# Kernel optimization log

Hardware: AMD Instinct MI355X
Metric: run time of the kernel (lower is better)

Reference implementation:

```python
import jax, jax.numpy as jnp
import numpy as np

N_NODES = 100000
N_EDGES = 800000
F_IN = 58


def setup_inputs() -> dict:
    key = jax.random.key(0)
    ks = jax.random.split(key, 8)
    x = jax.random.normal(ks[0], (N_NODES, F_IN), dtype=jnp.float32)
    edge_index = jax.random.randint(ks[1], (2, N_EDGES), 0, N_NODES, dtype=jnp.int64)

    def glorot(k, shape):
        fan_in = shape[-2]
        return jax.random.normal(k, shape, dtype=jnp.float32) * (1.0 / np.sqrt(fan_in))

    W1 = glorot(ks[2], (2, 58, 300))
    b1 = jnp.zeros((300,), jnp.float32)
    W2 = glorot(ks[3], (2, 300, 100))
    b2 = jnp.zeros((100,), jnp.float32)
    W3 = glorot(ks[4], (2, 100, 1))
    b3 = jnp.zeros((1,), jnp.float32)
    return {"x": x, "edge_index": edge_index, "W1": W1, "b1": b1,
            "W2": W2, "b2": b2, "W3": W3, "b3": b3}


def cheb_conv_k2(x, edge_index, W, b):
    """PyG ChebConv, K=2, sym normalization, lambda_max=2:
    L_hat = -D^{-1/2} A D^{-1/2}; out = x @ W[0] + (L_hat x) @ W[1] + b."""
    src, dst = edge_index[0], edge_index[1]
    n = x.shape[0]
    ones = jnp.ones(src.shape, x.dtype)
    deg = jax.ops.segment_sum(ones, src, num_segments=n)  # degree from row index
    dinv = jnp.where(deg > 0, 1.0 / jnp.sqrt(jnp.where(deg > 0, deg, 1.0)), 0.0)
    w = -(dinv[src] * dinv[dst])                          # [E] edge weights of L_hat
    tx1 = jax.ops.segment_sum(w[:, None] * x[src], dst, num_segments=n)  # [N,F]
    return x @ W[0] + tx1 @ W[1] + b


def reference(x, edge_index, W1, b1, W2, b2, W3, b3):
    # eval mode: dropout layers are identity
    h = jax.nn.relu(cheb_conv_k2(x, edge_index, W1, b1))
    h = jax.nn.relu(cheb_conv_k2(h, edge_index, W2, b2))
    return cheb_conv_k2(h, edge_index, W3, b3)
```

## Files before the change

### kernel.cpp

```cpp
#include <hip/hip_runtime.h>


typedef short bf16x8 __attribute__((ext_vector_type(8)));
typedef float f32x4 __attribute__((ext_vector_type(4)));

__device__ __forceinline__ unsigned f2bf(float f) {
  unsigned u = __float_as_uint(f);
  u += 0x7fff + ((u >> 16) & 1);
  return u >> 16;
}
__device__ __forceinline__ float bf2f(unsigned s) {
  return __uint_as_float(s << 16);
}

__global__ void k_count(const int* __restrict__ src, const int* __restrict__ dst,
                        unsigned* __restrict__ deg, unsigned* __restrict__ cnt,
                        unsigned* __restrict__ rank, int E) {
  int i = blockIdx.x * blockDim.x + threadIdx.x;
  if (i < E) {
    atomicAdd(&deg[src[i]], 1u);
    rank[i] = atomicAdd(&cnt[dst[i]], 1u);
  }
}

__global__ void k_dinv(const unsigned* __restrict__ deg, float* __restrict__ dinv, int N) {
  int i = blockIdx.x * blockDim.x + threadIdx.x;
  if (i < N) {
    unsigned d = deg[i];
    dinv[i] = d ? rsqrtf((float)d) : 0.0f;
  }
}

__global__ __launch_bounds__(256) void k_scan1(const unsigned* __restrict__ cnt,
                                               unsigned* __restrict__ btot, int N) {
  __shared__ unsigned s[256];
  int b = blockIdx.x, t = threadIdx.x;
  int base = b * 1024;
  unsigned sum = 0;
  for (int i = t; i < 1024; i += 256) {
    int idx = base + i;
    sum += (idx < N) ? cnt[idx] : 0u;
  }
  s[t] = sum;
  __syncthreads();
  for (int off = 128; off > 0; off >>= 1) {
    if (t < off) s[t] += s[t + off];
    __syncthreads();
  }
  if (t == 0) btot[b] = s[0];
}

__global__ __launch_bounds__(256) void k_scan2(unsigned* __restrict__ btot,
                                               unsigned* __restrict__ rowstart,
                                               int NB, int N, int E) {
  __shared__ unsigned s[256];
  int t = threadIdx.x;
  s[t] = (t < NB) ? btot[t] : 0u;
  __syncthreads();
  if (t == 0) {
    unsigned acc = 0;
    for (int i = 0; i < NB; i++) { unsigned v = s[i]; s[i] = acc; acc += v; }
  }
  __syncthreads();
  if (t < NB) btot[t] = s[t];
  if (t == 0) rowstart[N] = (unsigned)E;
}

__global__ __launch_bounds__(256) void k_scan3(const unsigned* __restrict__ cnt,
                                               const unsigned* __restrict__ btot,
                                               unsigned* __restrict__ rowstart, int N) {
  __shared__ unsigned ssum[256];
  int b = blockIdx.x, t = threadIdx.x;
  int base = b * 1024 + t * 4;
  unsigned v0 = 0, v1 = 0, v2 = 0, v3 = 0;
  if (base + 0 < N) v0 = cnt[base + 0];
  if (base + 1 < N) v1 = cnt[base + 1];
  if (base + 2 < N) v2 = cnt[base + 2];
  if (base + 3 < N) v3 = cnt[base + 3];
  ssum[t] = v0 + v1 + v2 + v3;
  __syncthreads();
  for (int off = 1; off < 256; off <<= 1) {
    unsigned add = (t >= off) ? ssum[t - off] : 0u;
    __syncthreads();
    ssum[t] += add;
    __syncthreads();
  }
  unsigned texcl = ((t == 0) ? 0u : ssum[t - 1]) + btot[b];
  unsigned r0 = texcl, r1 = r0 + v0, r2 = r1 + v1, r3 = r2 + v2;
  if (base + 0 < N) rowstart[base + 0] = r0;
  if (base + 1 < N) rowstart[base + 1] = r1;
  if (base + 2 < N) rowstart[base + 2] = r2;
  if (base + 3 < N) rowstart[base + 3] = r3;
}

__global__ void k_fill(const int* __restrict__ src, const int* __restrict__ dst,
                       const float* __restrict__ dinv, const unsigned* __restrict__ rowstart,
                       const unsigned* __restrict__ rank, int2* __restrict__ er, int E) {
  int e = blockIdx.x * blockDim.x + threadIdx.x;
  if (e >= E) return;
  int s = src[e], d = dst[e];
  er[rowstart[d] + rank[e]] = make_int2(s, __float_as_int(dinv[s]));
}

__global__ void k_prep_xb(const float* __restrict__ x, unsigned short* __restrict__ xb, int N) {
  int idx = blockIdx.x * blockDim.x + threadIdx.x;
  int n = idx >> 6, p = idx & 63;
  if (n >= N) return;
  int c = p * 2;
  if (c < 58) {
    unsigned lo = f2bf(x[(size_t)n * 58 + c]);
    unsigned hi = f2bf(x[(size_t)n * 58 + c + 1]);
    *(unsigned*)(xb + (size_t)n * 128 + c) = lo | (hi << 16);
  } else if (c >= 116) {
    *(unsigned*)(xb + (size_t)n * 128 + c) = 0;
  }
}

__global__ void k_prep_w1f(const float* __restrict__ W1, uint4* __restrict__ W1f) {
  int idx = blockIdx.x * blockDim.x + threadIdx.x;
  if (idx >= 4 * 20 * 64) return;
  int lane = idx & 63, j = (idx >> 6) % 20, s = (idx >> 6) / 20;
  int lr = lane & 15, g = lane >> 4;
  int c = j * 16 + lr;
  unsigned short v[8];
#pragma unroll
  for (int i = 0; i < 8; i++) {
    int k = s * 32 + g * 8 + i;
    float f = 0.0f;
    if (c < 300 && k < 116)
      f = (k < 58) ? W1[k * 300 + c] : W1[17400 + (k - 58) * 300 + c];
    v[i] = (unsigned short)f2bf(f);
  }
  W1f[idx] = *(const uint4*)v;
}

__global__ void k_prep_w2f(const float* __restrict__ W2, uint4* __restrict__ W2f) {
  int idx = blockIdx.x * blockDim.x + threadIdx.x;
  if (idx >= 10 * 13 * 64) return;
  int lane = idx & 63, j = (idx >> 6) % 13, s = (idx >> 6) / 13;
  int lr = lane & 15, g = lane >> 4;
  int r = j * 16 + lr;
  unsigned short v[8];
#pragma unroll
  for (int i = 0; i < 8; i++) {
    int k = s * 32 + g * 8 + i;
    float f = 0.0f;
    if (k < 300) {
      if (r < 100) f = W2[30000 + k * 100 + r];
      else if (r >= 104 && r < 204) f = W2[k * 100 + (r - 104)];
    }
    v[i] = (unsigned short)f2bf(f);
  }
  W2f[idx] = *(const uint4*)v;
}

__global__ void k_prep_b1pad(const float* __restrict__ b1, float* __restrict__ b1pad) {
  int t = blockIdx.x * blockDim.x + threadIdx.x;
  if (t < 320) b1pad[t] = (t < 300) ? b1[t] : 0.0f;
}

__global__ __launch_bounds__(256) void k_gather58(
    const unsigned* __restrict__ rowstart, const int2* __restrict__ er,
    const float* __restrict__ dinv, unsigned short* __restrict__ xb, int N) {
  int wid = (blockIdx.x * blockDim.x + threadIdx.x) >> 6;
  if (wid >= N) return;
  int lane = threadIdx.x & 63;
  int c0 = lane * 2;
  if (c0 >= 58) return;
  unsigned s0 = rowstart[wid], s1 = rowstart[wid + 1];
  float a0 = 0.f, a1 = 0.f, b0 = 0.f, b1 = 0.f;
  float c0a = 0.f, c1a = 0.f, d0 = 0.f, d1 = 0.f;
  unsigned e = s0;
  for (; e + 4 <= s1; e += 4) {
    int2 r0 = er[e], r1 = er[e + 1], r2 = er[e + 2], r3 = er[e + 3];
    unsigned v0 = *(const unsigned*)(xb + (size_t)r0.x * 128 + c0);
    unsigned v1 = *(const unsigned*)(xb + (size_t)r1.x * 128 + c0);
    unsigned v2 = *(const unsigned*)(xb + (size_t)r2.x * 128 + c0);
    unsigned v3 = *(const unsigned*)(xb + (size_t)r3.x * 128 + c0);
    float w0 = __int_as_float(r0.y), w1 = __int_as_float(r1.y);
    float w2 = __int_as_float(r2.y), w3 = __int_as_float(r3.y);
    a0 += w0 * bf2f(v0 & 0xffffu); a1 += w0 * bf2f(v0 >> 16);
    b0 += w1 * bf2f(v1 & 0xffffu); b1 += w1 * bf2f(v1 >> 16);
    c0a += w2 * bf2f(v2 & 0xffffu); c1a += w2 * bf2f(v2 >> 16);
    d0 += w3 * bf2f(v3 & 0xffffu); d1 += w3 * bf2f(v3 >> 16);
  }
  for (; e < s1; ++e) {
    int2 r = er[e];
    float w = __int_as_float(r.y);
    unsigned v = *(const unsigned*)(xb + (size_t)r.x * 128 + c0);
    a0 += w * bf2f(v & 0xffffu); a1 += w * bf2f(v >> 16);
  }
  float dd = -dinv[wid];
  float p0 = dd * ((a0 + b0) + (c0a + d0));
  float p1 = dd * ((a1 + b1) + (c1a + d1));
  *(unsigned*)(xb + (size_t)wid * 128 + 58 + c0) = f2bf(p0) | (f2bf(p1) << 16);
}

__global__ __launch_bounds__(256) void k_gather_l2(
    const unsigned* __restrict__ rowstart, const int2* __restrict__ er,
    const float* __restrict__ dinv, const unsigned short* __restrict__ ga2b,
    const float* __restrict__ b2, const float* __restrict__ W30,
    const float* __restrict__ W31, const float* __restrict__ b3,
    float* __restrict__ a3, float* __restrict__ g3, int N) {
  int wid = (blockIdx.x * blockDim.x + threadIdx.x) >> 6;
  if (wid >= N) return;
  int lane = threadIdx.x & 63;
  int c0 = lane * 2;
  bool act = c0 < 100;
  unsigned s0 = rowstart[wid], s1 = rowstart[wid + 1];
  float aa = 0.f, gg = 0.f;
  if (act) {
    float a0 = 0.f, a1 = 0.f, b0 = 0.f, b1 = 0.f;
    float c0a = 0.f, c1a = 0.f, d0 = 0.f, d1 = 0.f;
    unsigned e = s0;
    for (; e + 4 <= s1; e += 4) {
      int2 r0 = er[e], r1 = er[e + 1], r2 = er[e + 2], r3 = er[e + 3];
      unsigned v0 = *(const unsigned*)(ga2b + (size_t)r0.x * 208 + c0);
      unsigned v1 = *(const unsigned*)(ga2b + (size_t)r1.x * 208 + c0);
      unsigned v2 = *(const unsigned*)(ga2b + (size_t)r2.x * 208 + c0);
      unsigned v3 = *(const unsigned*)(ga2b + (size_t)r3.x * 208 + c0);
      float w0 = __int_as_float(r0.y), w1 = __int_as_float(r1.y);
      float w2 = __int_as_float(r2.y), w3 = __int_as_float(r3.y);
      a0 += w0 * bf2f(v0 & 0xffffu); a1 += w0 * bf2f(v0 >> 16);
      b0 += w1 * bf2f(v1 & 0xffffu); b1 += w1 * bf2f(v1 >> 16);
      c0a += w2 * bf2f(v2 & 0xffffu); c1a += w2 * bf2f(v2 >> 16);
      d0 += w3 * bf2f(v3 & 0xffffu); d1 += w3 * bf2f(v3 >> 16);
    }
    for (; e < s1; ++e) {
      int2 r = er[e];
      float w = __int_as_float(r.y);
      unsigned v = *(const unsigned*)(ga2b + (size_t)r.x * 208 + c0);
      a0 += w * bf2f(v & 0xffffu); a1 += w * bf2f(v >> 16);
    }
    float dd = -dinv[wid];
    float p0 = dd * ((a0 + b0) + (c0a + d0));
    float p1 = dd * ((a1 + b1) + (c1a + d1));
    unsigned av = *(const unsigned*)(ga2b + (size_t)wid * 208 + 104 + c0);
    float h0 = fmaxf(bf2f(av & 0xffffu) + p0 + b2[c0], 0.f);
    float h1 = fmaxf(bf2f(av >> 16) + p1 + b2[c0 + 1], 0.f);
    aa = h0 * W30[c0] + h1 * W30[c0 + 1];
    gg = h0 * W31[c0] + h1 * W31[c0 + 1];
  }
#pragma unroll
  for (int off = 32; off > 0; off >>= 1) {
    aa += __shfl_xor(aa, off);
    gg += __shfl_xor(gg, off);
  }
  if (lane == 0) {
    a3[wid] = aa + b3[0];
    g3[wid] = gg;
  }
}

__global__ void k_gather1(const unsigned* __restrict__ rowstart, const int2* __restrict__ er,
                          const float* __restrict__ dinv, const float* __restrict__ g3,
                          const float* __restrict__ a3, float* __restrict__ out, int N) {
  int n = blockIdx.x * blockDim.x + threadIdx.x;
  if (n >= N) return;
  unsigned s0 = rowstart[n], s1 = rowstart[n + 1];
  float a = 0.f, b = 0.f, c = 0.f, d = 0.f;
  unsigned e = s0;
  for (; e + 4 <= s1; e += 4) {
    int2 r0 = er[e], r1 = er[e + 1], r2 = er[e + 2], r3 = er[e + 3];
    float g0 = g3[r0.x], g1 = g3[r1.x], g2v = g3[r2.x], g3v = g3[r3.x];
    a += __int_as_float(r0.y) * g0;
    b += __int_as_float(r1.y) * g1;
    c += __int_as_float(r2.y) * g2v;
    d += __int_as_float(r3.y) * g3v;
  }
  for (; e < s1; ++e) {
    int2 r = er[e];
    a += __int_as_float(r.y) * g3[r.x];
  }
  out[n] = a3[n] - dinv[n] * ((a + b) + (c + d));
}

#define STG 324
__global__ __launch_bounds__(256, 3) void k_mm12_mfma(
    const unsigned short* __restrict__ xb, const uint4* __restrict__ W1f,
    const uint4* __restrict__ W2f, const float* __restrict__ b1pad,
    unsigned short* __restrict__ ga2b) {
  __shared__ unsigned short stage[4 * 16 * STG];
  int tid = threadIdx.x;
  int lane = tid & 63, wv = tid >> 6, lr = lane & 15, g = lane >> 4;
  int n0 = blockIdx.x * 64 + wv * 16;
  unsigned short* ost = stage + wv * 16 * STG;

  bf16x8 a1[4];
#pragma unroll
  for (int s = 0; s < 4; s++)
    a1[s] = *(const bf16x8*)(xb + (size_t)(n0 + lr) * 128 + s * 32 + g * 8);
#pragma unroll
  for (int half = 0; half < 2; half++) {
    f32x4 acc[10];
#pragma unroll
    for (int j = 0; j < 10; j++) acc[j] = (f32x4){0.f, 0.f, 0.f, 0.f};
#pragma unroll
    for (int s = 0; s < 4; s++) {
      bf16x8 w[10];
#pragma unroll
      for (int j = 0; j < 10; j++)
        w[j] = *(const bf16x8*)&W1f[(s * 20 + half * 10 + j) * 64 + lane];
      __builtin_amdgcn_sched_barrier(0);
#pragma unroll
      for (int j = 0; j < 10; j++)
        acc[j] = __builtin_amdgcn_mfma_f32_16x16x32_bf16(w[j], a1[s], acc[j], 0, 0, 0);
    }
#pragma unroll
    for (int j = 0; j < 10; j++) {
      int c = half * 160 + j * 16 + g * 4;
      float4 bv = *(const float4*)(b1pad + c);
      unsigned lo = f2bf(fmaxf(acc[j][0] + bv.x, 0.f)) |
                    (f2bf(fmaxf(acc[j][1] + bv.y, 0.f)) << 16);
      unsigned hi = f2bf(fmaxf(acc[j][2] + bv.z, 0.f)) |
                    (f2bf(fmaxf(acc[j][3] + bv.w, 0.f)) << 16);
      uint2 pk; pk.x = lo; pk.y = hi;
      *(uint2*)(ost + lr * STG + c) = pk;
    }
  }

  uint2 pk0[7], pk1[6];
  {
    f32x4 acc[7];
#pragma unroll
    for (int j = 0; j < 7; j++) acc[j] = (f32x4){0.f, 0.f, 0.f, 0.f};
#pragma unroll
    for (int s = 0; s < 10; s++) {
      bf16x8 a = *(const bf16x8*)(ost + lr * STG + s * 32 + g * 8);
      bf16x8 w[7];
#pragma unroll
      for (int j = 0; j < 7; j++) w[j] = *(const bf16x8*)&W2f[(s * 13 + j) * 64 + lane];
      __builtin_amdgcn_sched_barrier(0);
#pragma unroll
      for (int j = 0; j < 7; j++)
        acc[j] = __builtin_amdgcn_mfma_f32_16x16x32_bf16(w[j], a, acc[j], 0, 0, 0);
    }
#pragma unroll
    for (int j = 0; j < 7; j++) {
      pk0[j].x = f2bf(acc[j][0]) | (f2bf(acc[j][1]) << 16);
      pk0[j].y = f2bf(acc[j][2]) | (f2bf(acc[j][3]) << 16);
    }
  }
  {
    f32x4 acc[6];
#pragma unroll
    for (int j = 0; j < 6; j++) acc[j] = (f32x4){0.f, 0.f, 0.f, 0.f};
#pragma unroll
    for (int s = 0; s < 10; s++) {
      bf16x8 a = *(const bf16x8*)(ost + lr * STG + s * 32 + g * 8);
      bf16x8 w[6];
#pragma unroll
      for (int j = 0; j < 6; j++) w[j] = *(const bf16x8*)&W2f[(s * 13 + 7 + j) * 64 + lane];
      __builtin_amdgcn_sched_barrier(0);
#pragma unroll
      for (int j = 0; j < 6; j++)
        acc[j] = __builtin_amdgcn_mfma_f32_16x16x32_bf16(w[j], a, acc[j], 0, 0, 0);
    }
#pragma unroll
    for (int j = 0; j < 6; j++) {
      pk1[j].x = f2bf(acc[j][0]) | (f2bf(acc[j][1]) << 16);
      pk1[j].y = f2bf(acc[j][2]) | (f2bf(acc[j][3]) << 16);
    }
  }
#pragma unroll
  for (int j = 0; j < 7; j++)
    *(uint2*)(ost + lr * 216 + j * 16 + g * 4) = pk0[j];
#pragma unroll
  for (int j = 0; j < 6; j++)
    *(uint2*)(ost + lr * 216 + (7 + j) * 16 + g * 4) = pk1[j];
  uint4* gdst = (uint4*)(ga2b + (size_t)n0 * 208);
  for (int idx = lane; idx < 416; idx += 64) {
    int row = idx / 26, q = idx - row * 26;
    gdst[idx] = *(const uint4*)(ost + row * 216 + q * 8);
  }
}

extern "C" void kernel_launch(void* const* d_in, const int* in_sizes, int n_in,
                              void* d_out, int out_size, void* d_ws, size_t ws_size,
                              hipStream_t stream) {
  const float* x  = (const float*)d_in[0];
  const int*   ei = (const int*)d_in[1];
  const float* W1 = (const float*)d_in[2];
  const float* b1 = (const float*)d_in[3];
  const float* W2 = (const float*)d_in[4];
  const float* b2 = (const float*)d_in[5];
  const float* W3 = (const float*)d_in[6];
  const float* b3 = (const float*)d_in[7];
  float* out = (float*)d_out;

  const int N = in_sizes[0] / 58;
  const int E = in_sizes[1] / 2;
  const int NR = (N + 127) & ~127;
  const int NB = (N + 1023) / 1024;
  const int* src = ei;
  const int* dst = ei + E;

  char* ws = (char*)d_ws;
  size_t off = 0;
  auto alloc = [&](size_t bytes) -> void* {
    void* p = ws + off;
    off += (bytes + 255) & ~(size_t)255;
    return p;
  };
  unsigned* deg      = (unsigned*)alloc((size_t)2 * N * 4);
  unsigned* cnt      = deg + N;
  float*    dinv     = (float*)alloc((size_t)N * 4);
  unsigned* rowstart = (unsigned*)alloc((size_t)(N + 1) * 4);
  unsigned* rank     = (unsigned*)alloc((size_t)E * 4);
  unsigned* btot     = (unsigned*)alloc((size_t)256 * 4);
  int2*     er       = (int2*)alloc((size_t)E * 8);
  unsigned short* xb   = (unsigned short*)alloc((size_t)NR * 128 * 2);
  uint4*    W1f      = (uint4*)alloc((size_t)4 * 20 * 64 * 16);
  uint4*    W2f      = (uint4*)alloc((size_t)10 * 13 * 64 * 16);
  float*    b1pad    = (float*)alloc((size_t)320 * 4);
  unsigned short* ga2b = (unsigned short*)alloc((size_t)NR * 208 * 2);
  float* a3 = (float*)alloc((size_t)N * 4);
  float* g3 = (float*)alloc((size_t)N * 4);

  hipMemsetAsync(deg, 0, (size_t)2 * N * 4, stream);
  k_count<<<(E + 255) / 256, 256, 0, stream>>>(src, dst, deg, cnt, rank, E);
  k_dinv<<<(N + 255) / 256, 256, 0, stream>>>(deg, dinv, N);
  k_scan1<<<NB, 256, 0, stream>>>(cnt, btot, N);
  k_scan2<<<1, 256, 0, stream>>>(btot, rowstart, NB, N, E);
  k_scan3<<<NB, 256, 0, stream>>>(cnt, btot, rowstart, N);
  k_fill<<<(E + 255) / 256, 256, 0, stream>>>(src, dst, dinv, rowstart, rank, er, E);

  k_prep_w1f<<<(4 * 20 * 64 + 255) / 256, 256, 0, stream>>>(W1, W1f);
  k_prep_w2f<<<(10 * 13 * 64 + 255) / 256, 256, 0, stream>>>(W2, W2f);
  k_prep_b1pad<<<2, 256, 0, stream>>>(b1, b1pad);
  k_prep_xb<<<((size_t)N * 64 + 255) / 256, 256, 0, stream>>>(x, xb, N);

  k_gather58<<<(N + 3) / 4, 256, 0, stream>>>(rowstart, er, dinv, xb, N);
  k_mm12_mfma<<<NR / 64, 256, 0, stream>>>(xb, W1f, W2f, b1pad, ga2b);
  k_gather_l2<<<(N + 3) / 4, 256, 0, stream>>>(rowstart, er, dinv, ga2b,
                                               b2, W3, W3 + 100, b3, a3, g3, N);

  k_gather1<<<(N + 255) / 256, 256, 0, stream>>>(rowstart, er, dinv, g3, a3, out, N);
}
```

Before: 304.9 us.

## Fuse prep kernels into count launch, pack two nodes per wave, deepen gather unroll

The edge counting, x bf16 conversion, weight repacking and bias padding kernels are merged into one launch that dispatches on block ranges, removing several launch gaps. The 58-column gather now handles two nodes per 64-lane wave using half-waves, so fewer lanes sit idle. All three gather kernels switch to an 8-way unrolled edge loop with clamped indices and zeroed weights on the tail, giving more loads in flight per lane. The trade-offs are wasted loads on the padded tail slots and higher register pressure.

```diff
diff --git a/kernel.cpp b/kernel.cpp
--- a/kernel.cpp
+++ b/kernel.cpp
@@ -13,13 +13,81 @@
   return __uint_as_float(s << 16);
 }
 
-__global__ void k_count(const int* __restrict__ src, const int* __restrict__ dst,
-                        unsigned* __restrict__ deg, unsigned* __restrict__ cnt,
-                        unsigned* __restrict__ rank, int E) {
-  int i = blockIdx.x * blockDim.x + threadIdx.x;
-  if (i < E) {
-    atomicAdd(&deg[src[i]], 1u);
-    rank[i] = atomicAdd(&cnt[dst[i]], 1u);
+__global__ void k_count_prep(
+    const int* __restrict__ src, const int* __restrict__ dst,
+    unsigned* __restrict__ deg, unsigned* __restrict__ cnt,
+    unsigned* __restrict__ rank, int E, int EB,
+    const float* __restrict__ x, unsigned short* __restrict__ xb, int N, int XB,
+    const float* __restrict__ W1, uint4* __restrict__ W1f,
+    const float* __restrict__ W2, uint4* __restrict__ W2f,
+    const float* __restrict__ b1, float* __restrict__ b1pad) {
+  int b = blockIdx.x, t = threadIdx.x;
+  if (b < EB) {
+    int i = b * 256 + t;
+    if (i < E) {
+      atomicAdd(&deg[src[i]], 1u);
+      rank[i] = atomicAdd(&cnt[dst[i]], 1u);
+    }
+    return;
+  }
+  b -= EB;
+  if (b < XB) {
+    int idx = b * 256 + t;
+    int n = idx >> 6, p = idx & 63;
+    if (n >= N) return;
+    int c = p * 2;
+    if (c < 58) {
+      unsigned lo = f2bf(x[(size_t)n * 58 + c]);
+      unsigned hi = f2bf(x[(size_t)n * 58 + c + 1]);
+      *(unsigned*)(xb + (size_t)n * 128 + c) = lo | (hi << 16);
+    } else if (c >= 116) {
+      *(unsigned*)(xb + (size_t)n * 128 + c) = 0;
+    }
+    return;
+  }
+  b -= XB;
+  if (b < 20) {
+    int idx = b * 256 + t;
+    int lane = idx & 63, j = (idx >> 6) % 20, s = (idx >> 6) / 20;
+    int lr = lane & 15, g = lane >> 4;
+    int c = j * 16 + lr;
+    unsigned short v[8];
+#pragma unroll
+    for (int i = 0; i < 8; i++) {
+      int k = s * 32 + g * 8 + i;
+      float f = 0.0f;
+      if (c < 300 && k < 116)
+        f = (k < 58) ? W1[k * 300 + c] : W1[17400 + (k - 58) * 300 + c];
+      v[i] = (unsigned short)f2bf(f);
+    }
+    W1f[idx] = *(const uint4*)v;
+    return;
+  }
+  b -= 20;
+  if (b < 33) {
+    int idx = b * 256 + t;
+    if (idx >= 10 * 13 * 64) return;
+    int lane = idx & 63, j = (idx >> 6) % 13, s = (idx >> 6) / 13;
+    int lr = lane & 15, g = lane >> 4;
+    int r = j * 16 + lr;
+    unsigned short v[8];
+#pragma unroll
+    for (int i = 0; i < 8; i++) {
+      int k = s * 32 + g * 8 + i;
+      float f = 0.0f;
+      if (k < 300) {
+        if (r < 100) f = W2[30000 + k * 100 + r];
+        else if (r >= 104 && r < 204) f = W2[k * 100 + (r - 104)];
+      }
+      v[i] = (unsigned short)f2bf(f);
+    }
+    W2f[idx] = *(const uint4*)v;
+    return;
+  }
+  b -= 33;
+  {
+    int idx = b * 256 + t;
+    if (idx < 320) b1pad[idx] = (idx < 300) ? b1[idx] : 0.0f;
   }
 }
 
@@ -102,97 +170,39 @@
   er[rowstart[d] + rank[e]] = make_int2(s, __float_as_int(dinv[s]));
 }
 
-__global__ void k_prep_xb(const float* __restrict__ x, unsigned short* __restrict__ xb, int N) {
-  int idx = blockIdx.x * blockDim.x + threadIdx.x;
-  int n = idx >> 6, p = idx & 63;
-  if (n >= N) return;
-  int c = p * 2;
-  if (c < 58) {
-    unsigned lo = f2bf(x[(size_t)n * 58 + c]);
-    unsigned hi = f2bf(x[(size_t)n * 58 + c + 1]);
-    *(unsigned*)(xb + (size_t)n * 128 + c) = lo | (hi << 16);
-  } else if (c >= 116) {
-    *(unsigned*)(xb + (size_t)n * 128 + c) = 0;
-  }
-}
-
-__global__ void k_prep_w1f(const float* __restrict__ W1, uint4* __restrict__ W1f) {
-  int idx = blockIdx.x * blockDim.x + threadIdx.x;
-  if (idx >= 4 * 20 * 64) return;
-  int lane = idx & 63, j = (idx >> 6) % 20, s = (idx >> 6) / 20;
-  int lr = lane & 15, g = lane >> 4;
-  int c = j * 16 + lr;
-  unsigned short v[8];
-#pragma unroll
-  for (int i = 0; i < 8; i++) {
-    int k = s * 32 + g * 8 + i;
-    float f = 0.0f;
-    if (c < 300 && k < 116)
-      f = (k < 58) ? W1[k * 300 + c] : W1[17400 + (k - 58) * 300 + c];
-    v[i] = (unsigned short)f2bf(f);
-  }
-  W1f[idx] = *(const uint4*)v;
-}
-
-__global__ void k_prep_w2f(const float* __restrict__ W2, uint4* __restrict__ W2f) {
-  int idx = blockIdx.x * blockDim.x + threadIdx.x;
-  if (idx >= 10 * 13 * 64) return;
-  int lane = idx & 63, j = (idx >> 6) % 13, s = (idx >> 6) / 13;
-  int lr = lane & 15, g = lane >> 4;
-  int r = j * 16 + lr;
-  unsigned short v[8];
-#pragma unroll
-  for (int i = 0; i < 8; i++) {
-    int k = s * 32 + g * 8 + i;
-    float f = 0.0f;
-    if (k < 300) {
-      if (r < 100) f = W2[30000 + k * 100 + r];
-      else if (r >= 104 && r < 204) f = W2[k * 100 + (r - 104)];
-    }
-    v[i] = (unsigned short)f2bf(f);
-  }
-  W2f[idx] = *(const uint4*)v;
-}
-
-__global__ void k_prep_b1pad(const float* __restrict__ b1, float* __restrict__ b1pad) {
-  int t = blockIdx.x * blockDim.x + threadIdx.x;
-  if (t < 320) b1pad[t] = (t < 300) ? b1[t] : 0.0f;
-}
-
 __global__ __launch_bounds__(256) void k_gather58(
     const unsigned* __restrict__ rowstart, const int2* __restrict__ er,
     const float* __restrict__ dinv, unsigned short* __restrict__ xb, int N) {
-  int wid = (blockIdx.x * blockDim.x + threadIdx.x) >> 6;
-  if (wid >= N) return;
+  int pair = (blockIdx.x * blockDim.x + threadIdx.x) >> 6;
   int lane = threadIdx.x & 63;
-  int c0 = lane * 2;
-  if (c0 >= 58) return;
+  int wid = pair * 2 + (lane >> 5);
+  int c0 = (lane & 31) * 2;
+  if (wid >= N || c0 >= 58) return;
   unsigned s0 = rowstart[wid], s1 = rowstart[wid + 1];
-  float a0 = 0.f, a1 = 0.f, b0 = 0.f, b1 = 0.f;
-  float c0a = 0.f, c1a = 0.f, d0 = 0.f, d1 = 0.f;
-  unsigned e = s0;
-  for (; e + 4 <= s1; e += 4) {
-    int2 r0 = er[e], r1 = er[e + 1], r2 = er[e + 2], r3 = er[e + 3];
-    unsigned v0 = *(const unsigned*)(xb + (size_t)r0.x * 128 + c0);
-    unsigned v1 = *(const unsigned*)(xb + (size_t)r1.x * 128 + c0);
-    unsigned v2 = *(const unsigned*)(xb + (size_t)r2.x * 128 + c0);
-    unsigned v3 = *(const unsigned*)(xb + (size_t)r3.x * 128 + c0);
-    float w0 = __int_as_float(r0.y), w1 = __int_as_float(r1.y);
-    float w2 = __int_as_float(r2.y), w3 = __int_as_float(r3.y);
-    a0 += w0 * bf2f(v0 & 0xffffu); a1 += w0 * bf2f(v0 >> 16);
-    b0 += w1 * bf2f(v1 & 0xffffu); b1 += w1 * bf2f(v1 >> 16);
-    c0a += w2 * bf2f(v2 & 0xffffu); c1a += w2 * bf2f(v2 >> 16);
-    d0 += w3 * bf2f(v3 & 0xffffu); d1 += w3 * bf2f(v3 >> 16);
-  }
-  for (; e < s1; ++e) {
-    int2 r = er[e];
-    float w = __int_as_float(r.y);
-    unsigned v = *(const unsigned*)(xb + (size_t)r.x * 128 + c0);
-    a0 += w * bf2f(v & 0xffffu); a1 += w * bf2f(v >> 16);
+  float a0[8], a1[8];
+#pragma unroll
+  for (int k = 0; k < 8; k++) { a0[k] = 0.f; a1[k] = 0.f; }
+  for (unsigned e = s0; e < s1; e += 8) {
+    int2 r[8];
+#pragma unroll
+    for (int k = 0; k < 8; k++) {
+      unsigned idx = e + k;
+      r[k] = er[idx < s1 ? idx : s1 - 1];
+    }
+    unsigned v[8];
+#pragma unroll
+    for (int k = 0; k < 8; k++)
+      v[k] = *(const unsigned*)(xb + (size_t)r[k].x * 128 + c0);
+#pragma unroll
+    for (int k = 0; k < 8; k++) {
+      float w = (e + k < s1) ? __int_as_float(r[k].y) : 0.f;
+      a0[k] += w * bf2f(v[k] & 0xffffu);
+      a1[k] += w * bf2f(v[k] >> 16);
+    }
   }
   float dd = -dinv[wid];
-  float p0 = dd * ((a0 + b0) + (c0a + d0));
-  float p1 = dd * ((a1 + b1) + (c1a + d1));
+  float p0 = dd * (((a0[0] + a0[1]) + (a0[2] + a0[3])) + ((a0[4] + a0[5]) + (a0[6] + a0[7])));
+  float p1 = dd * (((a1[0] + a1[1]) + (a1[2] + a1[3])) + ((a1[4] + a1[5]) + (a1[6] + a1[7])));
   *(unsigned*)(xb + (size_t)wid * 128 + 58 + c0) = f2bf(p0) | (f2bf(p1) << 16);
 }
 
@@ -210,31 +220,30 @@
   unsigned s0 = rowstart[wid], s1 = rowstart[wid + 1];
   float aa = 0.f, gg = 0.f;
   if (act) {
-    float a0 = 0.f, a1 = 0.f, b0 = 0.f, b1 = 0.f;
-    float c0a = 0.f, c1a = 0.f, d0 = 0.f, d1 = 0.f;
-    unsigned e = s0;
-    for (; e + 4 <= s1; e += 4) {
-      int2 r0 = er[e], r1 = er[e + 1], r2 = er[e + 2], r3 = er[e + 3];
-      unsigned v0 = *(const unsigned*)(ga2b + (size_t)r0.x * 208 + c0);
-      unsigned v1 = *(const unsigned*)(ga2b + (size_t)r1.x * 208 + c0);
-      unsigned v2 = *(const unsigned*)(ga2b + (size_t)r2.x * 208 + c0);
-      unsigned v3 = *(const unsigned*)(ga2b + (size_t)r3.x * 208 + c0);
-      float w0 = __int_as_float(r0.y), w1 = __int_as_float(r1.y);
-      float w2 = __int_as_float(r2.y), w3 = __int_as_float(r3.y);
-      a0 += w0 * bf2f(v0 & 0xffffu); a1 += w0 * bf2f(v0 >> 16);
-      b0 += w1 * bf2f(v1 & 0xffffu); b1 += w1 * bf2f(v1 >> 16);
-      c0a += w2 * bf2f(v2 & 0xffffu); c1a += w2 * bf2f(v2 >> 16);
-      d0 += w3 * bf2f(v3 & 0xffffu); d1 += w3 * bf2f(v3 >> 16);
-    }
-    for (; e < s1; ++e) {
-      int2 r = er[e];
-      float w = __int_as_float(r.y);
-      unsigned v = *(const unsigned*)(ga2b + (size_t)r.x * 208 + c0);
-      a0 += w * bf2f(v & 0xffffu); a1 += w * bf2f(v >> 16);
+    float a0[8], a1[8];
+#pragma unroll
+    for (int k = 0; k < 8; k++) { a0[k] = 0.f; a1[k] = 0.f; }
+    for (unsigned e = s0; e < s1; e += 8) {
+      int2 r[8];
+#pragma unroll
+      for (int k = 0; k < 8; k++) {
+        unsigned idx = e + k;
+        r[k] = er[idx < s1 ? idx : s1 - 1];
+      }
+      unsigned v[8];
+#pragma unroll
+      for (int k = 0; k < 8; k++)
+        v[k] = *(const unsigned*)(ga2b + (size_t)r[k].x * 208 + c0);
+#pragma unroll
+      for (int k = 0; k < 8; k++) {
+        float w = (e + k < s1) ? __int_as_float(r[k].y) : 0.f;
+        a0[k] += w * bf2f(v[k] & 0xffffu);
+        a1[k] += w * bf2f(v[k] >> 16);
+      }
     }
     float dd = -dinv[wid];
-    float p0 = dd * ((a0 + b0) + (c0a + d0));
-    float p1 = dd * ((a1 + b1) + (c1a + d1));
+    float p0 = dd * (((a0[0] + a0[1]) + (a0[2] + a0[3])) + ((a0[4] + a0[5]) + (a0[6] + a0[7])));
+    float p1 = dd * (((a1[0] + a1[1]) + (a1[2] + a1[3])) + ((a1[4] + a1[5]) + (a1[6] + a1[7])));
     unsigned av = *(const unsigned*)(ga2b + (size_t)wid * 208 + 104 + c0);
     float h0 = fmaxf(bf2f(av & 0xffffu) + p0 + b2[c0], 0.f);
     float h1 = fmaxf(bf2f(av >> 16) + p1 + b2[c0 + 1], 0.f);
@@ -258,21 +267,27 @@
   int n = blockIdx.x * blockDim.x + threadIdx.x;
   if (n >= N) return;
   unsigned s0 = rowstart[n], s1 = rowstart[n + 1];
-  float a = 0.f, b = 0.f, c = 0.f, d = 0.f;
-  unsigned e = s0;
-  for (; e + 4 <= s1; e += 4) {
-    int2 r0 = er[e], r1 = er[e + 1], r2 = er[e + 2], r3 = er[e + 3];
-    float g0 = g3[r0.x], g1 = g3[r1.x], g2v = g3[r2.x], g3v = g3[r3.x];
-    a += __int_as_float(r0.y) * g0;
-    b += __int_as_float(r1.y) * g1;
-    c += __int_as_float(r2.y) * g2v;
-    d += __int_as_float(r3.y) * g3v;
-  }
-  for (; e < s1; ++e) {
-    int2 r = er[e];
-    a += __int_as_float(r.y) * g3[r.x];
-  }
-  out[n] = a3[n] - dinv[n] * ((a + b) + (c + d));
+  float a[8];
+#pragma unroll
+  for (int k = 0; k < 8; k++) a[k] = 0.f;
+  for (unsigned e = s0; e < s1; e += 8) {
+    int2 r[8];
+#pragma unroll
+    for (int k = 0; k < 8; k++) {
+      unsigned idx = e + k;
+      r[k] = er[idx < s1 ? idx : s1 - 1];
+    }
+    float gv[8];
+#pragma unroll
+    for (int k = 0; k < 8; k++) gv[k] = g3[r[k].x];
+#pragma unroll
+    for (int k = 0; k < 8; k++) {
+      float w = (e + k < s1) ? __int_as_float(r[k].y) : 0.f;
+      a[k] += w * gv[k];
+    }
+  }
+  float sum = ((a[0] + a[1]) + (a[2] + a[3])) + ((a[4] + a[5]) + (a[6] + a[7]));
+  out[n] = a3[n] - dinv[n] * sum;
 }
 
 #define STG 324
@@ -417,20 +432,19 @@
   float* a3 = (float*)alloc((size_t)N * 4);
   float* g3 = (float*)alloc((size_t)N * 4);
 
+  const int EB = (E + 255) / 256;
+  const int XB = ((size_t)N * 64 + 255) / 256;
+
   hipMemsetAsync(deg, 0, (size_t)2 * N * 4, stream);
-  k_count<<<(E + 255) / 256, 256, 0, stream>>>(src, dst, deg, cnt, rank, E);
+  k_count_prep<<<EB + XB + 20 + 33 + 2, 256, 0, stream>>>(
+      src, dst, deg, cnt, rank, E, EB, x, xb, N, XB, W1, W1f, W2, W2f, b1, b1pad);
   k_dinv<<<(N + 255) / 256, 256, 0, stream>>>(deg, dinv, N);
   k_scan1<<<NB, 256, 0, stream>>>(cnt, btot, N);
   k_scan2<<<1, 256, 0, stream>>>(btot, rowstart, NB, N, E);
   k_scan3<<<NB, 256, 0, stream>>>(cnt, btot, rowstart, N);
   k_fill<<<(E + 255) / 256, 256, 0, stream>>>(src, dst, dinv, rowstart, rank, er, E);
 
-  k_prep_w1f<<<(4 * 20 * 64 + 255) / 256, 256, 0, stream>>>(W1, W1f);
-  k_prep_w2f<<<(10 * 13 * 64 + 255) / 256, 256, 0, stream>>>(W2, W2f);
-  k_prep_b1pad<<<2, 256, 0, stream>>>(b1, b1pad);
-  k_prep_xb<<<((size_t)N * 64 + 255) / 256, 256, 0, stream>>>(x, xb, N);
-
-  k_gather58<<<(N + 3) / 4, 256, 0, stream>>>(rowstart, er, dinv, xb, N);
+  k_gather58<<<((N + 1) / 2 * 64 + 255) / 256, 256, 0, stream>>>(rowstart, er, dinv, xb, N);
   k_mm12_mfma<<<NR / 64, 256, 0, stream>>>(xb, W1f, W2f, b1pad, ga2b);
   k_gather_l2<<<(N + 3) / 4, 256, 0, stream>>>(rowstart, er, dinv, ga2b,
                                                b2, W3, W3 + 100, b3, a3, g3, N);
```

After: 271.0 us. -11.1%, faster.
